# Kernel tuning notes

Hardware: AMD Instinct MI355X
Metric: run time of the kernel (lower is better)

## Reference

```python
import jax, jax.numpy as jnp
import numpy as np

N_NODES = 100000
N_EDGES = 1600000
NFEAT = 128
NHID = 128


def setup_inputs() -> dict:
    key = jax.random.key(0)
    k1, k2, k3, k4 = jax.random.split(key, 4)
    x = jax.random.normal(k1, (N_NODES, NFEAT), dtype=jnp.float32)
    edge_index = jax.random.randint(k2, (2, N_EDGES), 0, N_NODES, dtype=jnp.int64)
    # GCNConv params (glorot-style scale)
    W1 = jax.random.normal(k3, (NFEAT, NHID), dtype=jnp.float32) * (1.0 / np.sqrt(NFEAT))
    b1 = jnp.zeros((NHID,), dtype=jnp.float32)
    return {"x": x, "edge_index": edge_index, "W1": W1, "b1": b1}


def gcn_conv(x, edge_index, W, b):
    # PyG GCNConv: out = D^{-1/2} (A + I) D^{-1/2} (x W) + b
    n = x.shape[0]
    loop = jnp.arange(n, dtype=edge_index.dtype)
    src = jnp.concatenate([edge_index[0], loop])  # message sources
    dst = jnp.concatenate([edge_index[1], loop])  # aggregation targets
    deg = jax.ops.segment_sum(jnp.ones_like(dst, dtype=x.dtype), dst, num_segments=n)
    dinv = jnp.where(deg > 0, jax.lax.rsqrt(deg), 0.0)
    norm = dinv[src] * dinv[dst]  # [E+N]
    h = x @ W  # [N, nhid]
    msg = h[src] * norm[:, None]  # gather + scale, [E+N, nhid]
    out = jax.ops.segment_sum(msg, dst, num_segments=n) + b
    return out


def reference(x, edge_index, W1, b1):
    # forward = gc1(x, edge_index) followed by dropout (identity in eval mode)
    return gcn_conv(x, edge_index, W1, b1)
```

## Files before the change

### kernel.cpp

```cpp
#include <hip/hip_runtime.h>
#include <math.h>


#define N_NODES 100000
#define N_EDGES 1600000
#define NF 128
#define LDW 136

#define BSHIFT 9
#define NBUCK 196
#define CHUNK 4096
#define NCHUNK 392
#define GEMM_BLOCKS 1563

typedef short bf16x8 __attribute__((ext_vector_type(8)));
typedef float f32x4  __attribute__((ext_vector_type(4)));
typedef unsigned short u16;

__device__ inline u16 f2bf(float f) {
    unsigned int u = __float_as_uint(f);
    return (u16)((u + 0x7fffu + ((u >> 16) & 1u)) >> 16);
}

__device__ inline f32x4 unpack4(unsigned int u) {
    f32x4 r;
    r[0] = (float)(signed char)(u & 0xff);
    r[1] = (float)(signed char)((u >> 8) & 0xff);
    r[2] = (float)(signed char)((u >> 16) & 0xff);
    r[3] = (float)(signed char)(u >> 24);
    return r;
}

__global__ __launch_bounds__(256) void fused1_kernel(const float* __restrict__ x,
                                                     const float* __restrict__ W,
                                                     signed char* __restrict__ h8,
                                                     float* __restrict__ rscale,
                                                     const int* __restrict__ ei,
                                                     int* __restrict__ histG,
                                                     int* __restrict__ bsum) {
    __shared__ u16 Wt[NF * LDW];
    __shared__ u16 xs[64 * LDW];
    const int t = threadIdx.x;

    if (blockIdx.x >= GEMM_BLOCKS) {
        int* hl = (int*)Wt;
        const int c = blockIdx.x - GEMM_BLOCKS;
        for (int b = t; b < NBUCK; b += 256) hl[b] = 0;
        __syncthreads();
        const int e0 = c * CHUNK;
        #pragma unroll 4
        for (int it = 0; it < CHUNK / 256; ++it) {
            int e = e0 + it * 256 + t;
            if (e < N_EDGES) atomicAdd(&hl[ei[N_EDGES + e] >> BSHIFT], 1);
        }
        __syncthreads();
        for (int b = t; b < NBUCK; b += 256) {
            int v = hl[b];
            histG[b * NCHUNK + c] = v;
            if (v) atomicAdd(&bsum[b], v);
        }
        return;
    }

    const int lane = t & 63;
    const int w = t >> 6;
    const int quad = lane >> 4;
    const int m = lane & 15;

    for (int idx = t; idx < NF * NF; idx += 256) {
        int k = idx >> 7, n = idx & 127;
        Wt[n * LDW + k] = f2bf(W[idx]);
    }

    const int rowbase = blockIdx.x * 64;
    for (int it = 0; it < 8; ++it) {
        int linear = it * 256 + t;
        int row = linear >> 5, colq = linear & 31;
        int grow = rowbase + row;
        float4 v = (grow < N_NODES) ? ((const float4*)x)[grow * 32 + colq]
                                    : make_float4(0.f, 0.f, 0.f, 0.f);
        u16* p = &xs[row * LDW + colq * 4];
        p[0] = f2bf(v.x); p[1] = f2bf(v.y); p[2] = f2bf(v.z); p[3] = f2bf(v.w);
    }
    __syncthreads();

    f32x4 acc[8];
    #pragma unroll
    for (int nt = 0; nt < 8; ++nt) acc[nt] = (f32x4){0.f, 0.f, 0.f, 0.f};

    const int r0 = w * 16;
    #pragma unroll
    for (int kt = 0; kt < 4; ++kt) {
        const int k0 = kt * 32;
        bf16x8 a = *(const bf16x8*)&xs[(r0 + m) * LDW + k0 + quad * 8];
        #pragma unroll
        for (int nt = 0; nt < 8; ++nt) {
            bf16x8 bb = *(const bf16x8*)&Wt[(nt * 16 + m) * LDW + k0 + quad * 8];
            acc[nt] = __builtin_amdgcn_mfma_f32_16x16x32_bf16(a, bb, acc[nt], 0, 0, 0);
        }
    }

    float rmax[4];
    #pragma unroll
    for (int r = 0; r < 4; ++r) {
        float mx = 0.f;
        #pragma unroll
        for (int nt = 0; nt < 8; ++nt) mx = fmaxf(mx, fabsf(acc[nt][r]));
        #pragma unroll
        for (int off = 1; off < 16; off <<= 1) mx = fmaxf(mx, __shfl_xor(mx, off));
        rmax[r] = fmaxf(mx, 1e-20f);
    }

    __syncthreads();
    char* xs8 = (char*)xs;
    #pragma unroll
    for (int r = 0; r < 4; ++r) {
        const float inv = 127.f / rmax[r];
        const int row = r0 + quad * 4 + r;
        #pragma unroll
        for (int nt = 0; nt < 8; ++nt) {
            int q = __float2int_rn(acc[nt][r] * inv);
            xs8[row * 144 + nt * 16 + m] = (char)q;
        }
        if (m == 0) {
            int grow = rowbase + row;
            if (grow < N_NODES) rscale[grow] = rmax[r] * (1.f / 127.f);
        }
    }
    __syncthreads();

    for (int it = 0; it < 2; ++it) {
        int linear = it * 256 + t;
        int row = linear >> 3, seg = linear & 7;
        int grow = rowbase + row;
        if (grow < N_NODES) {
            uint4 v = *(const uint4*)&xs8[row * 144 + seg * 16];
            ((uint4*)h8)[grow * 8 + seg] = v;
        }
    }
}

__global__ __launch_bounds__(256) void scanS2_kernel(const int* __restrict__ bsum,
                                                     int* __restrict__ bbase) {
    __shared__ int sb[256];
    const int t = threadIdx.x;
    int v = (t < NBUCK) ? bsum[t] : 0;
    sb[t] = v;
    __syncthreads();
    #pragma unroll
    for (int off = 1; off < 256; off <<= 1) {
        int cur = sb[t];
        int add = (t >= off) ? sb[t - off] : 0;
        __syncthreads();
        sb[t] = cur + add;
        __syncthreads();
    }
    if (t < NBUCK) bbase[t] = sb[t] - v;
    if (t == 0) bbase[NBUCK] = N_EDGES;
}

__global__ __launch_bounds__(256) void scanS3_kernel(int* __restrict__ histG,
                                                     const int* __restrict__ bbase) {
    __shared__ int lpair[256];
    const int t = threadIdx.x, b = blockIdx.x;
    int v0 = 0, v1 = 0;
    if (t < NCHUNK / 2) {
        v0 = histG[b * NCHUNK + 2 * t];
        v1 = histG[b * NCHUNK + 2 * t + 1];
    }
    int ps = v0 + v1;
    lpair[t] = ps;
    __syncthreads();
    #pragma unroll
    for (int off = 1; off < 256; off <<= 1) {
        int cur = lpair[t];
        int add = (t >= off) ? lpair[t - off] : 0;
        __syncthreads();
        lpair[t] = cur + add;
        __syncthreads();
    }
    if (t < NCHUNK / 2) {
        int base = bbase[b] + lpair[t] - ps;
        histG[b * NCHUNK + 2 * t] = base;
        histG[b * NCHUNK + 2 * t + 1] = base + v0;
    }
}

__global__ __launch_bounds__(256) void binB_kernel(const int* __restrict__ ei,
                                                   const int* __restrict__ histG,
                                                   unsigned int* __restrict__ ebuf) {
    __shared__ int lbase[NBUCK];
    __shared__ int lcur[NBUCK];
    const int t = threadIdx.x, c = blockIdx.x;
    for (int b = t; b < NBUCK; b += 256) { lbase[b] = histG[b * NCHUNK + c]; lcur[b] = 0; }
    __syncthreads();
    const int e0 = c * CHUNK;
    #pragma unroll 4
    for (int it = 0; it < CHUNK / 256; ++it) {
        int e = e0 + it * 256 + t;
        if (e < N_EDGES) {
            int s = ei[e];
            int d = ei[N_EDGES + e];
            int b = d >> BSHIFT;
            int r = atomicAdd(&lcur[b], 1);
            ebuf[lbase[b] + r] = ((unsigned)(d & 511) << 17) | (unsigned)s;
        }
    }
}

__global__ __launch_bounds__(256) void fill3_kernel(const unsigned int* __restrict__ ebuf,
                                                    const int* __restrict__ bbase,
                                                    const float* __restrict__ rscale,
                                                    int* __restrict__ rowptr,
                                                    float* __restrict__ dinv,
                                                    float* __restrict__ combo,
                                                    int* __restrict__ slot) {
    __shared__ int lcnt[1 << BSHIFT];
    __shared__ int lpair[256];
    __shared__ int lcur[1 << BSHIFT];
    const int t = threadIdx.x, b = blockIdx.x;
    const int n0 = b << BSHIFT;
    lcnt[t] = 0; lcnt[t + 256] = 0;
    __syncthreads();
    const int lo = bbase[b], hi = bbase[b + 1];
    for (int e = lo + t; e < hi; e += 256) {
        atomicAdd(&lcnt[ebuf[e] >> 17], 1);
    }
    __syncthreads();
    int c0 = lcnt[2 * t], c1 = lcnt[2 * t + 1];
    int ps = c0 + c1;
    lpair[t] = ps;
    __syncthreads();
    #pragma unroll
    for (int off = 1; off < 256; off <<= 1) {
        int v = lpair[t];
        int add = (t >= off) ? lpair[t - off] : 0;
        __syncthreads();
        lpair[t] = v + add;
        __syncthreads();
    }
    const int base = lo + lpair[t] - ps;
    lcur[2 * t] = base;
    lcur[2 * t + 1] = base + c0;
    const int n = n0 + 2 * t;
    if (n < N_NODES) {
        float dv = rsqrtf((float)c0 + 1.0f);
        rowptr[n] = base; dinv[n] = dv; combo[n] = dv * rscale[n];
    }
    if (n + 1 < N_NODES) {
        float dv = rsqrtf((float)c1 + 1.0f);
        rowptr[n + 1] = base + c0; dinv[n + 1] = dv; combo[n + 1] = dv * rscale[n + 1];
    }
    if (b == 0 && t == 0) rowptr[N_NODES] = N_EDGES;
    __syncthreads();
    for (int e = lo + t; e < hi; e += 256) {
        unsigned int p = ebuf[e];
        int pos = atomicAdd(&lcur[p >> 17], 1);
        slot[pos] = (int)(p & 0x1ffff);
    }
}

__global__ __launch_bounds__(256) void agg_kernel(const signed char* __restrict__ h8,
                                                  const float* __restrict__ dinv,
                                                  const float* __restrict__ combo,
                                                  const int* __restrict__ rowptr,
                                                  const int* __restrict__ slot,
                                                  const float* __restrict__ b,
                                                  float* __restrict__ out) {
    const int wave = threadIdx.x >> 6;
    const int lane = threadIdx.x & 63;
    const int i = blockIdx.x * 4 + wave;
    if (i >= N_NODES) return;

    const float di = dinv[i];
    const int start = rowptr[i];
    const int m = rowptr[i + 1] - start;
    const int half = lane >> 5;
    const int col = lane & 31;

    const unsigned int* h4 = (const unsigned int*)h8;
    f32x4 acc0 = {0.f, 0.f, 0.f, 0.f};
    f32x4 acc1 = {0.f, 0.f, 0.f, 0.f};

    for (int base = 0; base < m; base += 64) {
        const int mm = min(m - base, 64);
        int   s_l  = (lane < mm) ? slot[start + base + lane] : 0;
        float cw_l = (lane < mm) ? combo[s_l] : 0.0f;
        const int mu = (mm + 7) & ~7;
        for (int j = 0; j < mu; j += 8) {
            #pragma unroll
            for (int q = 0; q < 8; q += 2) {
                int   sj = __shfl(s_l, j + q + half);
                float wj = __shfl(cw_l, j + q + half) * di;
                unsigned int u = h4[sj * 32 + col];
                f32x4 hv = unpack4(u);
                if (q & 2) acc1 += hv * wj;
                else       acc0 += hv * wj;
            }
        }
    }

    f32x4 acc = acc0 + acc1;
    #pragma unroll
    for (int c = 0; c < 4; ++c) acc[c] += __shfl_xor(acc[c], 32);

    if (lane < 32) {
        float4 bb = ((const float4*)b)[col];
        unsigned int uv = h4[i * 32 + col];
        f32x4 hv = unpack4(uv);
        const float w0 = di * combo[i];
        float4 o;
        o.x = bb.x + acc[0] + w0 * hv[0];
        o.y = bb.y + acc[1] + w0 * hv[1];
        o.z = bb.z + acc[2] + w0 * hv[2];
        o.w = bb.w + acc[3] + w0 * hv[3];
        ((float4*)out)[i * 32 + col] = o;
    }
}

extern "C" void kernel_launch(void* const* d_in, const int* in_sizes, int n_in,
                              void* d_out, int out_size, void* d_ws, size_t ws_size,
                              hipStream_t stream) {
    const float* x  = (const float*)d_in[0];
    const int*   ei = (const int*)d_in[1];
    const float* W  = (const float*)d_in[2];
    const float* b  = (const float*)d_in[3];
    float* out = (float*)d_out;

    signed char* h8 = (signed char*)d_ws;
    float* rscale = (float*)d_ws + 3300000;
    float* dinv   = (float*)d_ws + 3400000;
    float* combo  = (float*)d_ws + 3500000;
    int*   rowptr = (int*)d_ws + 3600000;
    int*   bbase  = (int*)d_ws + 3750000;
    int*   bsum   = (int*)d_ws + 3760000;
    int*   histG  = (int*)d_ws + 3770000;
    int*   slot   = (int*)d_ws + 4000000;
    unsigned int* ebuf = (unsigned int*)d_ws + 5700000;

    hipMemsetAsync(bsum, 0, NBUCK * sizeof(int), stream);
    fused1_kernel<<<GEMM_BLOCKS + NCHUNK, 256, 0, stream>>>(x, W, h8, rscale,
                                                            ei, histG, bsum);
    scanS2_kernel<<<1, 256, 0, stream>>>(bsum, bbase);
    scanS3_kernel<<<NBUCK, 256, 0, stream>>>(histG, bbase);
    binB_kernel<<<NCHUNK, 256, 0, stream>>>(ei, histG, ebuf);
    fill3_kernel<<<NBUCK, 256, 0, stream>>>(ebuf, bbase, rscale, rowptr, dinv,
                                            combo, slot);
    agg_kernel<<<N_NODES / 4, 256, 0, stream>>>(h8, dinv, combo, rowptr, slot, b, out);
}
```

Measured before the change: 223.5 us.

## Replace two-level bucket sort with global degree atomics and direct CSR fill

Drops the chunk-histogram and bucket-binning passes. In-degrees are now counted with global atomics inside the fused GEMM kernel, a per-bucket scan builds rowptr and cursors, and edges are scattered straight into slot through global atomic cursors. W is converted to a bf16 shared-memory image once in a prep kernel, and int8 features are stored biased by 128 with a sum-of-weights correction. The aggregation now uses 16 lanes per edge with 8-byte loads. This removes launches and intermediate buffers, but adds contended global atomics and a non-deterministic edge order within each row.

```diff
diff --git a/kernel.cpp b/kernel.cpp
--- a/kernel.cpp
+++ b/kernel.cpp
@@ -12,6 +12,7 @@
 #define CHUNK 4096
 #define NCHUNK 392
 #define GEMM_BLOCKS 1563
+#define FILL_BLOCKS 1563
 
 typedef short bf16x8 __attribute__((ext_vector_type(8)));
 typedef float f32x4  __attribute__((ext_vector_type(4)));
@@ -22,24 +23,35 @@
     return (u16)((u + 0x7fffu + ((u >> 16) & 1u)) >> 16);
 }
 
-__device__ inline f32x4 unpack4(unsigned int u) {
+__device__ inline f32x4 unpk4u(unsigned int u) {
     f32x4 r;
-    r[0] = (float)(signed char)(u & 0xff);
-    r[1] = (float)(signed char)((u >> 8) & 0xff);
-    r[2] = (float)(signed char)((u >> 16) & 0xff);
-    r[3] = (float)(signed char)(u >> 24);
+    r[0] = (float)(u & 0xffu);
+    r[1] = (float)((u >> 8) & 0xffu);
+    r[2] = (float)((u >> 16) & 0xffu);
+    r[3] = (float)((u >> 24) & 0xffu);
     return r;
 }
 
+__global__ __launch_bounds__(256) void prep_kernel(const float* __restrict__ W,
+                                                   u16* __restrict__ Wimg,
+                                                   int* __restrict__ bsum) {
+    const int t = threadIdx.x;
+    if (blockIdx.x == 0 && t < NBUCK) bsum[t] = 0;
+    for (int idx = blockIdx.x * 256 + t; idx < NF * NF; idx += 16 * 256) {
+        int k = idx >> 7, n = idx & 127;
+        Wimg[n * LDW + k] = f2bf(W[idx]);
+    }
+}
+
 __global__ __launch_bounds__(256) void fused1_kernel(const float* __restrict__ x,
-                                                     const float* __restrict__ W,
+                                                     const u16* __restrict__ Wimg,
                                                      signed char* __restrict__ h8,
                                                      float* __restrict__ rscale,
                                                      const int* __restrict__ ei,
-                                                     int* __restrict__ histG,
+                                                     int* __restrict__ deg,
                                                      int* __restrict__ bsum) {
-    __shared__ u16 Wt[NF * LDW];
-    __shared__ u16 xs[64 * LDW];
+    __shared__ __align__(16) u16 Wt[NF * LDW];
+    __shared__ __align__(16) u16 xs[64 * LDW];
     const int t = threadIdx.x;
 
     if (blockIdx.x >= GEMM_BLOCKS) {
@@ -51,12 +63,15 @@
         #pragma unroll 4
         for (int it = 0; it < CHUNK / 256; ++it) {
             int e = e0 + it * 256 + t;
-            if (e < N_EDGES) atomicAdd(&hl[ei[N_EDGES + e] >> BSHIFT], 1);
+            if (e < N_EDGES) {
+                int d = ei[N_EDGES + e];
+                atomicAdd(&hl[d >> BSHIFT], 1);
+                atomicAdd(&deg[d], 1);
+            }
         }
         __syncthreads();
         for (int b = t; b < NBUCK; b += 256) {
             int v = hl[b];
-            histG[b * NCHUNK + c] = v;
             if (v) atomicAdd(&bsum[b], v);
         }
         return;
@@ -67,10 +82,8 @@
     const int quad = lane >> 4;
     const int m = lane & 15;
 
-    for (int idx = t; idx < NF * NF; idx += 256) {
-        int k = idx >> 7, n = idx & 127;
-        Wt[n * LDW + k] = f2bf(W[idx]);
-    }
+    for (int idx = t; idx < (NF * LDW * 2) / 16; idx += 256)
+        ((uint4*)Wt)[idx] = ((const uint4*)Wimg)[idx];
 
     const int rowbase = blockIdx.x * 64;
     for (int it = 0; it < 8; ++it) {
@@ -79,8 +92,9 @@
         int grow = rowbase + row;
         float4 v = (grow < N_NODES) ? ((const float4*)x)[grow * 32 + colq]
                                     : make_float4(0.f, 0.f, 0.f, 0.f);
-        u16* p = &xs[row * LDW + colq * 4];
-        p[0] = f2bf(v.x); p[1] = f2bf(v.y); p[2] = f2bf(v.z); p[3] = f2bf(v.w);
+        unsigned a0 = (unsigned)f2bf(v.x) | ((unsigned)f2bf(v.y) << 16);
+        unsigned a1 = (unsigned)f2bf(v.z) | ((unsigned)f2bf(v.w) << 16);
+        *(uint2*)&xs[row * LDW + colq * 4] = make_uint2(a0, a1);
     }
     __syncthreads();
 
@@ -119,7 +133,7 @@
         const int row = r0 + quad * 4 + r;
         #pragma unroll
         for (int nt = 0; nt < 8; ++nt) {
-            int q = __float2int_rn(acc[nt][r] * inv);
+            int q = __float2int_rn(acc[nt][r] * inv) + 128;
             xs8[row * 144 + nt * 16 + m] = (char)q;
         }
         if (m == 0) {
@@ -140,10 +154,17 @@
     }
 }
 
-__global__ __launch_bounds__(256) void scanS2_kernel(const int* __restrict__ bsum,
-                                                     int* __restrict__ bbase) {
+__global__ __launch_bounds__(256) void sK_kernel(const int* __restrict__ bsum,
+                                                 const int* __restrict__ deg,
+                                                 const float* __restrict__ rscale,
+                                                 int* __restrict__ rowptr,
+                                                 int* __restrict__ cursor,
+                                                 float* __restrict__ dinv,
+                                                 float* __restrict__ combo) {
     __shared__ int sb[256];
-    const int t = threadIdx.x;
+    __shared__ int lpair[256];
+    const int t = threadIdx.x, bkt = blockIdx.x;
+
     int v = (t < NBUCK) ? bsum[t] : 0;
     sb[t] = v;
     __syncthreads();
@@ -155,20 +176,13 @@
         sb[t] = cur + add;
         __syncthreads();
     }
-    if (t < NBUCK) bbase[t] = sb[t] - v;
-    if (t == 0) bbase[NBUCK] = N_EDGES;
-}
-
-__global__ __launch_bounds__(256) void scanS3_kernel(int* __restrict__ histG,
-                                                     const int* __restrict__ bbase) {
-    __shared__ int lpair[256];
-    const int t = threadIdx.x, b = blockIdx.x;
-    int v0 = 0, v1 = 0;
-    if (t < NCHUNK / 2) {
-        v0 = histG[b * NCHUNK + 2 * t];
-        v1 = histG[b * NCHUNK + 2 * t + 1];
-    }
-    int ps = v0 + v1;
+    const int bb = (bkt > 0) ? sb[bkt - 1] : 0;
+
+    const int n0 = bkt << BSHIFT;
+    const int na = n0 + 2 * t, nb = na + 1;
+    int c0 = (na < N_NODES) ? deg[na] : 0;
+    int c1 = (nb < N_NODES) ? deg[nb] : 0;
+    int ps = c0 + c1;
     lpair[t] = ps;
     __syncthreads();
     #pragma unroll
@@ -179,84 +193,33 @@
         lpair[t] = cur + add;
         __syncthreads();
     }
-    if (t < NCHUNK / 2) {
-        int base = bbase[b] + lpair[t] - ps;
-        histG[b * NCHUNK + 2 * t] = base;
-        histG[b * NCHUNK + 2 * t + 1] = base + v0;
-    }
-}
-
-__global__ __launch_bounds__(256) void binB_kernel(const int* __restrict__ ei,
-                                                   const int* __restrict__ histG,
-                                                   unsigned int* __restrict__ ebuf) {
-    __shared__ int lbase[NBUCK];
-    __shared__ int lcur[NBUCK];
-    const int t = threadIdx.x, c = blockIdx.x;
-    for (int b = t; b < NBUCK; b += 256) { lbase[b] = histG[b * NCHUNK + c]; lcur[b] = 0; }
-    __syncthreads();
-    const int e0 = c * CHUNK;
+    const int base = bb + lpair[t] - ps;
+    if (na < N_NODES) {
+        rowptr[na] = base; cursor[na] = base;
+        float dv = rsqrtf((float)c0 + 1.0f);
+        dinv[na] = dv; combo[na] = dv * rscale[na];
+    }
+    if (nb < N_NODES) {
+        rowptr[nb] = base + c0; cursor[nb] = base + c0;
+        float dv = rsqrtf((float)c1 + 1.0f);
+        dinv[nb] = dv; combo[nb] = dv * rscale[nb];
+    }
+    if (bkt == 0 && t == 0) rowptr[N_NODES] = N_EDGES;
+}
+
+__global__ __launch_bounds__(256) void fill_kernel(const int* __restrict__ ei,
+                                                   int* __restrict__ cursor,
+                                                   int* __restrict__ slot) {
+    const int e0 = blockIdx.x * 1024 + threadIdx.x;
     #pragma unroll 4
-    for (int it = 0; it < CHUNK / 256; ++it) {
-        int e = e0 + it * 256 + t;
+    for (int it = 0; it < 4; ++it) {
+        int e = e0 + it * 256;
         if (e < N_EDGES) {
             int s = ei[e];
             int d = ei[N_EDGES + e];
-            int b = d >> BSHIFT;
-            int r = atomicAdd(&lcur[b], 1);
-            ebuf[lbase[b] + r] = ((unsigned)(d & 511) << 17) | (unsigned)s;
-        }
-    }
-}
-
-__global__ __launch_bounds__(256) void fill3_kernel(const unsigned int* __restrict__ ebuf,
-                                                    const int* __restrict__ bbase,
-                                                    const float* __restrict__ rscale,
-                                                    int* __restrict__ rowptr,
-                                                    float* __restrict__ dinv,
-                                                    float* __restrict__ combo,
-                                                    int* __restrict__ slot) {
-    __shared__ int lcnt[1 << BSHIFT];
-    __shared__ int lpair[256];
-    __shared__ int lcur[1 << BSHIFT];
-    const int t = threadIdx.x, b = blockIdx.x;
-    const int n0 = b << BSHIFT;
-    lcnt[t] = 0; lcnt[t + 256] = 0;
-    __syncthreads();
-    const int lo = bbase[b], hi = bbase[b + 1];
-    for (int e = lo + t; e < hi; e += 256) {
-        atomicAdd(&lcnt[ebuf[e] >> 17], 1);
-    }
-    __syncthreads();
-    int c0 = lcnt[2 * t], c1 = lcnt[2 * t + 1];
-    int ps = c0 + c1;
-    lpair[t] = ps;
-    __syncthreads();
-    #pragma unroll
-    for (int off = 1; off < 256; off <<= 1) {
-        int v = lpair[t];
-        int add = (t >= off) ? lpair[t - off] : 0;
-        __syncthreads();
-        lpair[t] = v + add;
-        __syncthreads();
-    }
-    const int base = lo + lpair[t] - ps;
-    lcur[2 * t] = base;
-    lcur[2 * t + 1] = base + c0;
-    const int n = n0 + 2 * t;
-    if (n < N_NODES) {
-        float dv = rsqrtf((float)c0 + 1.0f);
-        rowptr[n] = base; dinv[n] = dv; combo[n] = dv * rscale[n];
-    }
-    if (n + 1 < N_NODES) {
-        float dv = rsqrtf((float)c1 + 1.0f);
-        rowptr[n + 1] = base + c0; dinv[n + 1] = dv; combo[n + 1] = dv * rscale[n + 1];
-    }
-    if (b == 0 && t == 0) rowptr[N_NODES] = N_EDGES;
-    __syncthreads();
-    for (int e = lo + t; e < hi; e += 256) {
-        unsigned int p = ebuf[e];
-        int pos = atomicAdd(&lcur[p >> 17], 1);
-        slot[pos] = (int)(p & 0x1ffff);
+            int pos = atomicAdd(&cursor[d], 1);
+            slot[pos] = s;
+        }
     }
 }
 
@@ -275,46 +238,65 @@
     const float di = dinv[i];
     const int start = rowptr[i];
     const int m = rowptr[i + 1] - start;
-    const int half = lane >> 5;
-    const int col = lane & 31;
-
-    const unsigned int* h4 = (const unsigned int*)h8;
-    f32x4 acc0 = {0.f, 0.f, 0.f, 0.f};
-    f32x4 acc1 = {0.f, 0.f, 0.f, 0.f};
+    const int quad = lane >> 4;
+    const int qcol = lane & 15;
+
+    const uint2* h16 = (const uint2*)h8;
+    f32x4 a0lo = {0.f, 0.f, 0.f, 0.f}, a0hi = {0.f, 0.f, 0.f, 0.f};
+    f32x4 a1lo = {0.f, 0.f, 0.f, 0.f}, a1hi = {0.f, 0.f, 0.f, 0.f};
+    float ws = 0.f;
 
     for (int base = 0; base < m; base += 64) {
         const int mm = min(m - base, 64);
         int   s_l  = (lane < mm) ? slot[start + base + lane] : 0;
         float cw_l = (lane < mm) ? combo[s_l] : 0.0f;
-        const int mu = (mm + 7) & ~7;
-        for (int j = 0; j < mu; j += 8) {
+        const int mu = (mm + 15) & ~15;
+        for (int j = 0; j < mu; j += 16) {
             #pragma unroll
-            for (int q = 0; q < 8; q += 2) {
-                int   sj = __shfl(s_l, j + q + half);
-                float wj = __shfl(cw_l, j + q + half) * di;
-                unsigned int u = h4[sj * 32 + col];
-                f32x4 hv = unpack4(u);
-                if (q & 2) acc1 += hv * wj;
-                else       acc0 += hv * wj;
+            for (int q = 0; q < 16; q += 4) {
+                int   sj = __shfl(s_l,  j + q + quad);
+                float wj = __shfl(cw_l, j + q + quad);
+                uint2 u  = h16[sj * 16 + qcol];
+                ws += wj;
+                f32x4 lo = unpk4u(u.x);
+                f32x4 hi = unpk4u(u.y);
+                if (q & 4) { a1lo += lo * wj; a1hi += hi * wj; }
+                else       { a0lo += lo * wj; a0hi += hi * wj; }
             }
         }
     }
 
-    f32x4 acc = acc0 + acc1;
-    #pragma unroll
-    for (int c = 0; c < 4; ++c) acc[c] += __shfl_xor(acc[c], 32);
-
-    if (lane < 32) {
-        float4 bb = ((const float4*)b)[col];
-        unsigned int uv = h4[i * 32 + col];
-        f32x4 hv = unpack4(uv);
-        const float w0 = di * combo[i];
-        float4 o;
-        o.x = bb.x + acc[0] + w0 * hv[0];
-        o.y = bb.y + acc[1] + w0 * hv[1];
-        o.z = bb.z + acc[2] + w0 * hv[2];
-        o.w = bb.w + acc[3] + w0 * hv[3];
-        ((float4*)out)[i * 32 + col] = o;
+    #pragma unroll
+    for (int c = 0; c < 4; ++c) { a0lo[c] += a1lo[c]; a0hi[c] += a1hi[c]; }
+    #pragma unroll
+    for (int c = 0; c < 4; ++c) {
+        a0lo[c] += __shfl_xor(a0lo[c], 16);
+        a0hi[c] += __shfl_xor(a0hi[c], 16);
+        a0lo[c] += __shfl_xor(a0lo[c], 32);
+        a0hi[c] += __shfl_xor(a0hi[c], 32);
+    }
+    ws += __shfl_xor(ws, 16);
+    ws += __shfl_xor(ws, 32);
+
+    if (lane < 16) {
+        const float ci = combo[i];
+        uint2 us = h16[i * 16 + lane];
+        f32x4 slo = unpk4u(us.x);
+        f32x4 shi = unpk4u(us.y);
+        const float corr = 128.f * (ws + ci);
+        float4 bb0 = ((const float4*)b)[lane * 2];
+        float4 bb1 = ((const float4*)b)[lane * 2 + 1];
+        float4 o0, o1;
+        o0.x = bb0.x + di * (a0lo[0] + ci * slo[0] - corr);
+        o0.y = bb0.y + di * (a0lo[1] + ci * slo[1] - corr);
+        o0.z = bb0.z + di * (a0lo[2] + ci * slo[2] - corr);
+        o0.w = bb0.w + di * (a0lo[3] + ci * slo[3] - corr);
+        o1.x = bb1.x + di * (a0hi[0] + ci * shi[0] - corr);
+        o1.y = bb1.y + di * (a0hi[1] + ci * shi[1] - corr);
+        o1.z = bb1.z + di * (a0hi[2] + ci * shi[2] - corr);
+        o1.w = bb1.w + di * (a0hi[3] + ci * shi[3] - corr);
+        ((float4*)out)[i * 32 + lane * 2] = o0;
+        ((float4*)out)[i * 32 + lane * 2 + 1] = o1;
     }
 }
 
@@ -332,19 +314,18 @@
     float* dinv   = (float*)d_ws + 3400000;
     float* combo  = (float*)d_ws + 3500000;
     int*   rowptr = (int*)d_ws + 3600000;
-    int*   bbase  = (int*)d_ws + 3750000;
-    int*   bsum   = (int*)d_ws + 3760000;
-    int*   histG  = (int*)d_ws + 3770000;
-    int*   slot   = (int*)d_ws + 4000000;
-    unsigned int* ebuf = (unsigned int*)d_ws + 5700000;
-
-    hipMemsetAsync(bsum, 0, NBUCK * sizeof(int), stream);
-    fused1_kernel<<<GEMM_BLOCKS + NCHUNK, 256, 0, stream>>>(x, W, h8, rscale,
-                                                            ei, histG, bsum);
-    scanS2_kernel<<<1, 256, 0, stream>>>(bsum, bbase);
-    scanS3_kernel<<<NBUCK, 256, 0, stream>>>(histG, bbase);
-    binB_kernel<<<NCHUNK, 256, 0, stream>>>(ei, histG, ebuf);
-    fill3_kernel<<<NBUCK, 256, 0, stream>>>(ebuf, bbase, rscale, rowptr, dinv,
-                                            combo, slot);
+    int*   cursor = (int*)d_ws + 3750000;
+    int*   bsum   = (int*)d_ws + 3900000;
+    int*   deg    = (int*)d_ws + 3950000;
+    u16*   Wimg   = (u16*)((int*)d_ws + 4100000);
+    int*   slot   = (int*)d_ws + 4200000;
+
+    hipMemsetAsync(deg, 0, N_NODES * sizeof(int), stream);
+    prep_kernel<<<16, 256, 0, stream>>>(W, Wimg, bsum);
+    fused1_kernel<<<GEMM_BLOCKS + NCHUNK, 256, 0, stream>>>(x, Wimg, h8, rscale,
+                                                            ei, deg, bsum);
+    sK_kernel<<<NBUCK, 256, 0, stream>>>(bsum, deg, rscale, rowptr, cursor,
+                                         dinv, combo);
+    fill_kernel<<<FILL_BLOCKS, 256, 0, stream>>>(ei, cursor, slot);
     agg_kernel<<<N_NODES / 4, 256, 0, stream>>>(h8, dinv, combo, rowptr, slot, b, out);
 }
```

Measured after the change: 371.8 us. 1.66x slower.
